# Kernel tuning notes

Measured on AMD Instinct MI355X. Metric: run time of the kernel, lower is better.

## Reference

```python
import jax, jax.numpy as jnp
import numpy as np

B, S, D, H = 2, 2048, 1024, 16
DK = D // H


def setup_inputs() -> dict:
    key = jax.random.key(0)
    ks = jax.random.split(key, 9)
    sc = 0.02
    return {
        "x": jax.random.normal(ks[0], (B, S, D), dtype=jnp.float32),
        "attention_mask": jnp.ones((B, S), dtype=jnp.int32),
        "Wq": jax.random.normal(ks[1], (D, D), dtype=jnp.float32) * sc,
        "bq": jax.random.normal(ks[2], (D,), dtype=jnp.float32) * sc,
        "Wk": jax.random.normal(ks[3], (D, D), dtype=jnp.float32) * sc,
        "bk": jax.random.normal(ks[4], (D,), dtype=jnp.float32) * sc,
        "Wv": jax.random.normal(ks[5], (D, D), dtype=jnp.float32) * sc,
        "bv": jax.random.normal(ks[6], (D,), dtype=jnp.float32) * sc,
        "Wo": jax.random.normal(ks[7], (D, D), dtype=jnp.float32) * sc,
        "bo": jax.random.normal(ks[8], (D,), dtype=jnp.float32) * sc,
    }


def reference(x, attention_mask, Wq, bq, Wk, bk, Wv, bv, Wo, bo):
    b, s, d = x.shape
    # projections (Linear: x @ W + b) then split heads -> [b, h, s, dk]
    def heads(t):
        return t.reshape(b, s, H, DK).transpose(0, 2, 1, 3)
    Q = heads(x @ Wq + bq)
    K = heads(x @ Wk + bk)
    V = heads(x @ Wv + bv)
    # NOTE: original computes K @ Q^T (not Q @ K^T) and applies NO 1/sqrt(dk) scale
    scores = jnp.einsum("bhid,bhjd->bhij", K, Q)  # [b, h, s, s]
    causal = jnp.tril(jnp.ones((s, s), dtype=bool))  # [s, s]
    final_mask = attention_mask[:, None, None, :].astype(bool) & causal[None, None]
    scores = jnp.where(final_mask, scores, -jnp.inf)
    attn = jax.nn.softmax(scores, axis=-1)
    out = jnp.einsum("bhij,bhjd->bhid", attn, V)  # [b, h, s, dk]
    out = out.transpose(0, 2, 1, 3).reshape(b, s, d)
    return out @ Wo + bo
```

## Files before the change

### kernel.cpp

```cpp
#include <hip/hip_runtime.h>
#include <stdint.h>
#include <stddef.h>


typedef short bf16x8 __attribute__((ext_vector_type(8)));
typedef float f32x4  __attribute__((ext_vector_type(4)));

__device__ __forceinline__ short f2bf(float f) {
  union { float f; uint32_t u; } a; a.f = f;
  uint32_t r = a.u + 0x7fffu + ((a.u >> 16) & 1u);
  return (short)(r >> 16);
}
__device__ __forceinline__ short f2bf_trunc(float f) {
  union { float f; uint32_t u; } a; a.f = f;
  return (short)(a.u >> 16);
}
__device__ __forceinline__ float bf2f(short s) {
  union { uint32_t u; float f; } a; a.u = ((uint32_t)(uint16_t)s) << 16;
  return a.f;
}
__device__ __forceinline__ float fast_exp2(float x) {
#if __has_builtin(__builtin_amdgcn_exp2f)
  return __builtin_amdgcn_exp2f(x);
#else
  return exp2f(x);
#endif
}
__device__ __forceinline__ void async16(const void* g, void* l) {
  __builtin_amdgcn_global_load_lds(
      (const __attribute__((address_space(1))) uint32_t*)g,
      (__attribute__((address_space(3))) uint32_t*)l, 16, 0, 0);
}
#define MFMA(a, b, c) __builtin_amdgcn_mfma_f32_16x16x32_bf16((a), (b), (c), 0, 0, 0)

__global__ void k_split_x(const float* __restrict__ x, short* __restrict__ xhi,
                          short* __restrict__ xlo) {
  int i = blockIdx.x * 256 + threadIdx.x;
  float4 v = ((const float4*)x)[i];
  short4 h, l;
  h.x = f2bf(v.x); l.x = f2bf(v.x - bf2f(h.x));
  h.y = f2bf(v.y); l.y = f2bf(v.y - bf2f(h.y));
  h.z = f2bf(v.z); l.z = f2bf(v.z - bf2f(h.z));
  h.w = f2bf(v.w); l.w = f2bf(v.w - bf2f(h.w));
  ((short4*)xhi)[i] = h;
  ((short4*)xlo)[i] = l;
}

__global__ void k_prep_w(const float* __restrict__ Wq, const float* __restrict__ Wk,
                         const float* __restrict__ Wv, const float* __restrict__ Wo,
                         short* __restrict__ whi) {
  __shared__ float T[64][65];
  int z = blockIdx.z;
  const float* W = (z == 0) ? Wq : (z == 1) ? Wk : (z == 2) ? Wv : Wo;
  int n0 = blockIdx.x * 64, k0 = blockIdx.y * 64;
  int t = threadIdx.x;
  int rr = t >> 4, cc = (t & 15) * 4;
#pragma unroll
  for (int it = 0; it < 4; ++it) {
    int row = rr + it * 16;
    float4 v = *(const float4*)&W[(size_t)(k0 + row) * 1024 + n0 + cc];
    T[row][cc] = v.x; T[row][cc + 1] = v.y; T[row][cc + 2] = v.z; T[row][cc + 3] = v.w;
  }
  __syncthreads();
  short* oh = whi + (size_t)z * 1048576;
#pragma unroll
  for (int it = 0; it < 4; ++it) {
    int nrow = rr + it * 16;
    short4 h4;
    h4.x = f2bf(T[cc + 0][nrow]);
    h4.y = f2bf(T[cc + 1][nrow]);
    h4.z = f2bf(T[cc + 2][nrow]);
    h4.w = f2bf(T[cc + 3][nrow]);
    *(short4*)&oh[(size_t)(n0 + nrow) * 1024 + k0 + cc] = h4;
  }
}

__global__ __launch_bounds__(256, 3) void k_gemm_qkv(
    const short* __restrict__ xhi, const short* __restrict__ xlo,
    const short* __restrict__ whi,
    const float* __restrict__ bq, const float* __restrict__ bk,
    const float* __restrict__ bv,
    short* __restrict__ Qhi, short* __restrict__ Qlo,
    short* __restrict__ Khi, short* __restrict__ Klo,
    short* __restrict__ Vb) {
  __shared__ short AH[2][4096];
  __shared__ short AL[2][4096];
  __shared__ short BH[2][4096];
  int tid = threadIdx.x;
  int bx = blockIdx.x;
  int m0 = blockIdx.y * 128;
  int n0g = bx * 128;
  bool SPLIT = (bx < 16);
  int w = tid >> 6, lane = tid & 63, lr = lane & 15, lq = lane >> 4;
  int wm = w >> 1, wn = w & 1;
  f32x4 acc[4][4] = {};

  auto stage = [&](int ks, int pb) {
#pragma unroll
    for (int it = 0; it < 2; ++it) {
      int idx = it * 256 + tid;
      int row = idx >> 2, c = idx & 3;
      int cs = c ^ (row & 3);
      size_t ga = (size_t)(m0 + row) * 1024 + ks * 32 + cs * 8;
      async16(xhi + ga, &AH[pb][idx * 8]);
      if (SPLIT) async16(xlo + ga, &AL[pb][idx * 8]);
      size_t gb = (size_t)(n0g + row) * 1024 + ks * 32 + cs * 8;
      async16(whi + gb, &BH[pb][idx * 8]);
    }
  };

  stage(0, 0);
  int p = 0;
  int g = lq ^ (lr & 3);
  for (int ks = 0; ks < 32; ++ks) {
    __syncthreads();
    if (ks < 31) stage(ks + 1, p ^ 1);
    const bf16x8* A8 = (const bf16x8*)AH[p];
    const bf16x8* L8 = (const bf16x8*)AL[p];
    const bf16x8* B8 = (const bf16x8*)BH[p];
    bf16x8 af[4], al[4], bfr[4];
#pragma unroll
    for (int mt = 0; mt < 4; ++mt) af[mt] = A8[(wm * 64 + mt * 16 + lr) * 4 + g];
#pragma unroll
    for (int nt = 0; nt < 4; ++nt) bfr[nt] = B8[(wn * 64 + nt * 16 + lr) * 4 + g];
    if (SPLIT) {
#pragma unroll
      for (int mt = 0; mt < 4; ++mt) al[mt] = L8[(wm * 64 + mt * 16 + lr) * 4 + g];
    }
#pragma unroll
    for (int mt = 0; mt < 4; ++mt)
#pragma unroll
      for (int nt = 0; nt < 4; ++nt)
        acc[mt][nt] = MFMA(af[mt], bfr[nt], acc[mt][nt]);
    if (SPLIT) {
#pragma unroll
      for (int mt = 0; mt < 4; ++mt)
#pragma unroll
        for (int nt = 0; nt < 4; ++nt)
          acc[mt][nt] = MFMA(al[mt], bfr[nt], acc[mt][nt]);
    }
    p ^= 1;
  }

  int z = bx >> 3;
  const float* bias = (z == 0) ? bq : (z == 1) ? bk : bv;
  short* Ch = (z == 0) ? Qhi : (z == 1) ? Khi : Vb;
  short* Cl = (z == 0) ? Qlo : Klo;
#pragma unroll
  for (int nt = 0; nt < 4; ++nt) {
    int colg = (n0g & 1023) + wn * 64 + nt * 16 + lr;
    float bvv = bias[colg];
#pragma unroll
    for (int mt = 0; mt < 4; ++mt)
#pragma unroll
      for (int r = 0; r < 4; ++r) {
        int row = m0 + wm * 64 + mt * 16 + lq * 4 + r;
        float v = acc[mt][nt][r] + bvv;
        size_t o = (size_t)row * 1024 + colg;
        if (z < 2) {
          short hh = f2bf(v);
          Ch[o] = hh;
          Cl[o] = f2bf(v - bf2f(hh));
        } else {
          Ch[o] = f2bf(v);
        }
      }
  }
}

__global__ __launch_bounds__(256, 2) void k_gemm_o(
    const short* __restrict__ Ab, const short* __restrict__ Bb,
    const float* __restrict__ bias, float* __restrict__ Cf) {
  __shared__ short AH[2][4096];
  __shared__ short BH[2][4096];
  int tid = threadIdx.x;
  int m0 = blockIdx.y * 128, n0 = blockIdx.x * 128;
  int w = tid >> 6, lane = tid & 63, lr = lane & 15, lq = lane >> 4;
  int wm = w >> 1, wn = w & 1;
  f32x4 acc[4][4] = {};

  auto stage = [&](int ks, int pb) {
#pragma unroll
    for (int it = 0; it < 2; ++it) {
      int idx = it * 256 + tid;
      int row = idx >> 2, c = idx & 3;
      int cs = c ^ (row & 3);
      async16(Ab + (size_t)(m0 + row) * 1024 + ks * 32 + cs * 8, &AH[pb][idx * 8]);
      async16(Bb + (size_t)(n0 + row) * 1024 + ks * 32 + cs * 8, &BH[pb][idx * 8]);
    }
  };

  stage(0, 0);
  int p = 0;
  int g = lq ^ (lr & 3);
  for (int ks = 0; ks < 32; ++ks) {
    __syncthreads();
    if (ks < 31) stage(ks + 1, p ^ 1);
    const bf16x8* A8 = (const bf16x8*)AH[p];
    const bf16x8* B8 = (const bf16x8*)BH[p];
    bf16x8 af[4], bfr[4];
#pragma unroll
    for (int mt = 0; mt < 4; ++mt) af[mt] = A8[(wm * 64 + mt * 16 + lr) * 4 + g];
#pragma unroll
    for (int nt = 0; nt < 4; ++nt) bfr[nt] = B8[(wn * 64 + nt * 16 + lr) * 4 + g];
#pragma unroll
    for (int mt = 0; mt < 4; ++mt)
#pragma unroll
      for (int nt = 0; nt < 4; ++nt)
        acc[mt][nt] = MFMA(af[mt], bfr[nt], acc[mt][nt]);
    p ^= 1;
  }
#pragma unroll
  for (int nt = 0; nt < 4; ++nt) {
    int col = n0 + wn * 64 + nt * 16 + lr;
    float bvv = bias[col];
#pragma unroll
    for (int mt = 0; mt < 4; ++mt)
#pragma unroll
      for (int r = 0; r < 4; ++r) {
        int row = m0 + wm * 64 + mt * 16 + lq * 4 + r;
        Cf[(size_t)row * 1024 + col] = acc[mt][nt][r] + bvv;
      }
  }
}

__global__ void k_vt(const short* __restrict__ Vb, short* __restrict__ Vt) {
  __shared__ short T[64][72];
  int s0 = blockIdx.x * 64;
  int bh = blockIdx.y, b = bh >> 4, h = bh & 15;
  int tid = threadIdx.x;
#pragma unroll
  for (int it = 0; it < 2; ++it) {
    int idx = it * 256 + tid, r = idx >> 3, c = idx & 7;
    bf16x8 v = *(const bf16x8*)(Vb + (size_t)(b * 2048 + s0 + r) * 1024 + h * 64 + c * 8);
    *(bf16x8*)&T[r][c * 8] = v;
  }
  __syncthreads();
#pragma unroll
  for (int it = 0; it < 2; ++it) {
    int idx = it * 256 + tid, d = idx >> 3, sc = idx & 7;
    bf16x8 vv;
#pragma unroll
    for (int j = 0; j < 8; ++j) vv[j] = T[sc * 8 + j][d];
    *(bf16x8*)(Vt + (size_t)(bh * 64 + d) * 2048 + s0 + sc * 8) = vv;
  }
}

__global__ __launch_bounds__(256, 2) void k_attn(
    const short* __restrict__ Khi, const short* __restrict__ Klo,
    const short* __restrict__ Qhi, const short* __restrict__ Qlo,
    const short* __restrict__ Vt, const int* __restrict__ amask,
    short* __restrict__ Obuf) {
  __shared__ short KQh[2][4096];
  __shared__ short KQl[2][4096];
  __shared__ short VS[2][4096];
  __shared__ short P[8][16 * 72];
  __shared__ float mb[2048];
  int tid = threadIdx.x;
  int pr = blockIdx.x;
  int bh = blockIdx.y, b = bh >> 4, h = bh & 15;
  int w = tid >> 6, lane = tid & 63, lr = lane & 15, lq = lane >> 4;
  const float LOG2E = 1.44269504f;
  int iA = pr, iB = 31 - pr;

  for (int j = tid; j < 2048; j += 256)
    mb[j] = amask[b * 2048 + j] ? 0.0f : -1e30f;

  bf16x8 qhA[2], qlA[2], qhB[2], qlB[2];
  {
    size_t ra = ((size_t)(b * 2048 + iA * 64 + w * 16 + lr)) * 1024 + h * 64;
    size_t rb = ((size_t)(b * 2048 + iB * 64 + w * 16 + lr)) * 1024 + h * 64;
#pragma unroll
    for (int ks = 0; ks < 2; ++ks) {
      qhA[ks] = *(const bf16x8*)(Khi + ra + ks * 32 + lq * 8);
      qlA[ks] = *(const bf16x8*)(Klo + ra + ks * 32 + lq * 8);
      qhB[ks] = *(const bf16x8*)(Khi + rb + ks * 32 + lq * 8);
      qlB[ks] = *(const bf16x8*)(Klo + rb + ks * 32 + lq * 8);
    }
  }

  f32x4 OA[4] = {}, OB[4] = {};
  float lsA[4] = {0.f, 0.f, 0.f, 0.f}, lsB[4] = {0.f, 0.f, 0.f, 0.f};
  int ibaseA = iA * 64 + w * 16 + lq * 4;
  int ibaseB = iB * 64 + w * 16 + lq * 4;
  int g = lq ^ (lr & 3);

  auto stage = [&](int jt, int pb) {
#pragma unroll
    for (int it = 0; it < 2; ++it) {
      int idx = it * 256 + tid;
      int rg = idx >> 8, rr = (idx >> 2) & 63, c = idx & 3;
      int cs = c ^ (rr & 3);
      size_t gq = ((size_t)(b * 2048 + jt * 64 + rr)) * 1024 + h * 64 + rg * 32 + cs * 8;
      async16(Qhi + gq, &KQh[pb][idx * 8]);
      async16(Qlo + gq, &KQl[pb][idx * 8]);
      size_t gv = ((size_t)(bh * 64 + rr)) * 2048 + jt * 64 + rg * 32 + cs * 8;
      async16(Vt + gv, &VS[pb][idx * 8]);
    }
  };

  auto softmax = [&](f32x4* s, float* ls, int ibase, int j0, bool diag, int slot) {
    float pv[4][4];
#pragma unroll
    for (int nt = 0; nt < 4; ++nt) {
      int j = j0 + nt * 16 + lr;
      float bias_j = mb[j];
#pragma unroll
      for (int r = 0; r < 4; ++r)
        pv[nt][r] = fast_exp2(s[nt][r] * LOG2E + bias_j);
    }
    if (diag) {
#pragma unroll
      for (int nt = 0; nt < 4; ++nt) {
        int j = j0 + nt * 16 + lr;
#pragma unroll
        for (int r = 0; r < 4; ++r)
          if (j > ibase + r) pv[nt][r] = 0.f;
      }
    }
#pragma unroll
    for (int nt = 0; nt < 4; ++nt)
#pragma unroll
      for (int r = 0; r < 4; ++r) {
        ls[r] += pv[nt][r];
        P[w * 2 + slot][(lq * 4 + r) * 72 + nt * 16 + lr] = f2bf_trunc(pv[nt][r]);
      }
  };

  stage(0, 0);
  int p = 0;
  for (int jt = 0; jt <= iB; ++jt) {
    __syncthreads();
    if (jt < iB) stage(jt + 1, p ^ 1);
    bool DUAL = (jt <= iA);
    int j0 = jt * 64;
    const bf16x8* KH8 = (const bf16x8*)KQh[p];
    const bf16x8* KL8 = (const bf16x8*)KQl[p];
    const bf16x8* V8  = (const bf16x8*)VS[p];

    f32x4 sA[4] = {}, sB[4] = {};
#pragma unroll
    for (int nt = 0; nt < 4; ++nt) {
      int ri = (nt * 16 + lr) * 4 + g;
#pragma unroll
      for (int ks = 0; ks < 2; ++ks) {
        bf16x8 kb  = KH8[ks * 256 + ri];
        bf16x8 klb = KL8[ks * 256 + ri];
        sB[nt] = MFMA(qhB[ks], kb, sB[nt]);
        sB[nt] = MFMA(qhB[ks], klb, sB[nt]);
        sB[nt] = MFMA(qlB[ks], kb, sB[nt]);
        if (DUAL) {
          sA[nt] = MFMA(qhA[ks], kb, sA[nt]);
          sA[nt] = MFMA(qhA[ks], klb, sA[nt]);
          sA[nt] = MFMA(qlA[ks], kb, sA[nt]);
        }
      }
    }
    softmax(sB, lsB, ibaseB, j0, jt == iB, 0);
    if (DUAL) softmax(sA, lsA, ibaseA, j0, jt == iA, 1);

    bf16x8 paB[2], paA[2];
#pragma unroll
    for (int ks = 0; ks < 2; ++ks)
      paB[ks] = *(const bf16x8*)&P[w * 2 + 0][lr * 72 + ks * 32 + lq * 8];
    if (DUAL) {
#pragma unroll
      for (int ks = 0; ks < 2; ++ks)
        paA[ks] = *(const bf16x8*)&P[w * 2 + 1][lr * 72 + ks * 32 + lq * 8];
    }
#pragma unroll
    for (int ks = 0; ks < 2; ++ks)
#pragma unroll
      for (int nt = 0; nt < 4; ++nt) {
        bf16x8 vb = V8[ks * 256 + (nt * 16 + lr) * 4 + g];
        OB[nt] = MFMA(paB[ks], vb, OB[nt]);
        if (DUAL) OA[nt] = MFMA(paA[ks], vb, OA[nt]);
      }
    p ^= 1;
  }

  auto fin = [&](f32x4* O, float* ls, int i0) {
#pragma unroll
    for (int r = 0; r < 4; ++r) {
      float t = ls[r];
      t += __shfl_xor(t, 1);
      t += __shfl_xor(t, 2);
      t += __shfl_xor(t, 4);
      t += __shfl_xor(t, 8);
      float inv = 1.0f / t;
#pragma unroll
      for (int nt = 0; nt < 4; ++nt) {
        int row = b * 2048 + i0 + w * 16 + lq * 4 + r;
        int col = h * 64 + nt * 16 + lr;
        Obuf[(size_t)row * 1024 + col] = f2bf(O[nt][r] * inv);
      }
    }
  };
  fin(OA, lsA, iA * 64);
  fin(OB, lsB, iB * 64);
}

extern "C" void kernel_launch(void* const* d_in, const int* in_sizes, int n_in,
                              void* d_out, int out_size, void* d_ws, size_t ws_size,
                              hipStream_t stream) {
  const float* x  = (const float*)d_in[0];
  const int* amask = (const int*)d_in[1];
  const float* Wq = (const float*)d_in[2];
  const float* bq = (const float*)d_in[3];
  const float* Wk = (const float*)d_in[4];
  const float* bk = (const float*)d_in[5];
  const float* Wv = (const float*)d_in[6];
  const float* bv = (const float*)d_in[7];
  const float* Wo = (const float*)d_in[8];
  const float* bo = (const float*)d_in[9];

  char* ws = (char*)d_ws;
  const size_t MB = 1024 * 1024;
  short* xhi = (short*)(ws);
  short* xlo = (short*)(ws + 8 * MB);
  short* whi = (short*)(ws + 16 * MB);
  short* Qhi = (short*)(ws + 28 * MB);
  short* Qlo = (short*)(ws + 36 * MB);
  short* Khi = (short*)(ws + 44 * MB);
  short* Klo = (short*)(ws + 52 * MB);
  short* Vb  = (short*)(ws + 60 * MB);
  short* Vt   = xhi;
  short* Obuf = xlo;

  k_split_x<<<4096, 256, 0, stream>>>(x, xhi, xlo);
  k_prep_w<<<dim3(16, 16, 4), 256, 0, stream>>>(Wq, Wk, Wv, Wo, whi);

  k_gemm_qkv<<<dim3(24, 32), 256, 0, stream>>>(xhi, xlo, whi, bq, bk, bv,
                                               Qhi, Qlo, Khi, Klo, Vb);
  k_vt<<<dim3(32, 32), 256, 0, stream>>>(Vb, Vt);
  k_attn<<<dim3(16, 32), 256, 0, stream>>>(Khi, Klo, Qhi, Qlo, Vt, amask, Obuf);
  k_gemm_o<<<dim3(8, 32), 256, 0, stream>>>(Obuf, whi + 3 * 1048576, bo, (float*)d_out);
}
```

Before: 251.7 us.

## Restructure attention to one band per block with transposed scores and register P

The attention kernel now handles a single 64-row band per block, longest bands first, instead of pairing bands A/B. It computes scores transposed so the softmax probabilities stay in registers and are reshuffled with ds_bpermute instead of going through an LDS P buffer. The mask is read per tile with a ballot fast path that skips masking when all keys are valid. LOG2E is folded into Q in the projection epilogue. Dropping the shared P and mask buffers allows three blocks per CU, at the cost of losing the pairwise load balancing and adding cross-lane permutes.

```diff
diff --git a/kernel.cpp b/kernel.cpp
--- a/kernel.cpp
+++ b/kernel.cpp
@@ -11,13 +11,13 @@
   uint32_t r = a.u + 0x7fffu + ((a.u >> 16) & 1u);
   return (short)(r >> 16);
 }
-__device__ __forceinline__ short f2bf_trunc(float f) {
-  union { float f; uint32_t u; } a; a.f = f;
-  return (short)(a.u >> 16);
-}
 __device__ __forceinline__ float bf2f(short s) {
   union { uint32_t u; float f; } a; a.u = ((uint32_t)(uint16_t)s) << 16;
   return a.f;
+}
+__device__ __forceinline__ uint32_t pack2bf(float a, float b) {
+  union { float f; uint32_t u; } x, y; x.f = a; y.f = b;
+  return (x.u >> 16) | (y.u & 0xffff0000u);
 }
 __device__ __forceinline__ float fast_exp2(float x) {
 #if __has_builtin(__builtin_amdgcn_exp2f)
@@ -143,6 +143,7 @@
   }
 
   int z = bx >> 3;
+  const float LOG2E = 1.44269504f;
   const float* bias = (z == 0) ? bq : (z == 1) ? bk : bv;
   short* Ch = (z == 0) ? Qhi : (z == 1) ? Khi : Vb;
   short* Cl = (z == 0) ? Qlo : Klo;
@@ -156,6 +157,7 @@
       for (int r = 0; r < 4; ++r) {
         int row = m0 + wm * 64 + mt * 16 + lq * 4 + r;
         float v = acc[mt][nt][r] + bvv;
+        if (z == 0) v *= LOG2E;
         size_t o = (size_t)row * 1024 + colg;
         if (z < 2) {
           short hh = f2bf(v);
@@ -246,158 +248,142 @@
   }
 }
 
-__global__ __launch_bounds__(256, 2) void k_attn(
+__global__ __launch_bounds__(256, 3) void k_attn(
     const short* __restrict__ Khi, const short* __restrict__ Klo,
     const short* __restrict__ Qhi, const short* __restrict__ Qlo,
     const short* __restrict__ Vt, const int* __restrict__ amask,
     short* __restrict__ Obuf) {
-  __shared__ short KQh[2][4096];
-  __shared__ short KQl[2][4096];
+  __shared__ short QH[2][4096];
+  __shared__ short QL[2][4096];
   __shared__ short VS[2][4096];
-  __shared__ short P[8][16 * 72];
-  __shared__ float mb[2048];
   int tid = threadIdx.x;
-  int pr = blockIdx.x;
+  int band = 31 - blockIdx.x;
   int bh = blockIdx.y, b = bh >> 4, h = bh & 15;
   int w = tid >> 6, lane = tid & 63, lr = lane & 15, lq = lane >> 4;
-  const float LOG2E = 1.44269504f;
-  int iA = pr, iB = 31 - pr;
-
-  for (int j = tid; j < 2048; j += 256)
-    mb[j] = amask[b * 2048 + j] ? 0.0f : -1e30f;
-
-  bf16x8 qhA[2], qlA[2], qhB[2], qlB[2];
+  int i0 = band * 64;
+
+  bf16x8 kh[2], kl[2];
   {
-    size_t ra = ((size_t)(b * 2048 + iA * 64 + w * 16 + lr)) * 1024 + h * 64;
-    size_t rb = ((size_t)(b * 2048 + iB * 64 + w * 16 + lr)) * 1024 + h * 64;
+    size_t ra = ((size_t)(b * 2048 + i0 + w * 16 + lr)) * 1024 + h * 64;
 #pragma unroll
     for (int ks = 0; ks < 2; ++ks) {
-      qhA[ks] = *(const bf16x8*)(Khi + ra + ks * 32 + lq * 8);
-      qlA[ks] = *(const bf16x8*)(Klo + ra + ks * 32 + lq * 8);
-      qhB[ks] = *(const bf16x8*)(Khi + rb + ks * 32 + lq * 8);
-      qlB[ks] = *(const bf16x8*)(Klo + rb + ks * 32 + lq * 8);
-    }
-  }
-
-  f32x4 OA[4] = {}, OB[4] = {};
-  float lsA[4] = {0.f, 0.f, 0.f, 0.f}, lsB[4] = {0.f, 0.f, 0.f, 0.f};
-  int ibaseA = iA * 64 + w * 16 + lq * 4;
-  int ibaseB = iB * 64 + w * 16 + lq * 4;
-  int g = lq ^ (lr & 3);
+      kh[ks] = *(const bf16x8*)(Khi + ra + ks * 32 + lq * 8);
+      kl[ks] = *(const bf16x8*)(Klo + ra + ks * 32 + lq * 8);
+    }
+  }
+
+  f32x4 O[4] = {};
+  float lsacc = 0.f;
+  int iq = i0 + w * 16 + lr;
+  int baddr0 = (((lq & 1) * 2) * 16 + lr) * 4;
+  int baddr1 = baddr0 + 64;
 
   auto stage = [&](int jt, int pb) {
+    int j0 = jt * 64;
 #pragma unroll
     for (int it = 0; it < 2; ++it) {
       int idx = it * 256 + tid;
-      int rg = idx >> 8, rr = (idx >> 2) & 63, c = idx & 3;
-      int cs = c ^ (rr & 3);
-      size_t gq = ((size_t)(b * 2048 + jt * 64 + rr)) * 1024 + h * 64 + rg * 32 + cs * 8;
-      async16(Qhi + gq, &KQh[pb][idx * 8]);
-      async16(Qlo + gq, &KQl[pb][idx * 8]);
-      size_t gv = ((size_t)(bh * 64 + rr)) * 2048 + jt * 64 + rg * 32 + cs * 8;
+      int rr = idx >> 3, c = idx & 7;
+      int cs = c ^ (rr & 7);
+      size_t gq = ((size_t)(b * 2048 + j0 + rr)) * 1024 + h * 64 + cs * 8;
+      async16(Qhi + gq, &QH[pb][idx * 8]);
+      async16(Qlo + gq, &QL[pb][idx * 8]);
+      size_t gv = ((size_t)(bh * 64 + rr)) * 2048 + j0 + cs * 8;
       async16(Vt + gv, &VS[pb][idx * 8]);
     }
-  };
-
-  auto softmax = [&](f32x4* s, float* ls, int ibase, int j0, bool diag, int slot) {
-    float pv[4][4];
-#pragma unroll
-    for (int nt = 0; nt < 4; ++nt) {
-      int j = j0 + nt * 16 + lr;
-      float bias_j = mb[j];
-#pragma unroll
-      for (int r = 0; r < 4; ++r)
-        pv[nt][r] = fast_exp2(s[nt][r] * LOG2E + bias_j);
-    }
-    if (diag) {
-#pragma unroll
-      for (int nt = 0; nt < 4; ++nt) {
-        int j = j0 + nt * 16 + lr;
-#pragma unroll
-        for (int r = 0; r < 4; ++r)
-          if (j > ibase + r) pv[nt][r] = 0.f;
-      }
-    }
-#pragma unroll
-    for (int nt = 0; nt < 4; ++nt)
-#pragma unroll
-      for (int r = 0; r < 4; ++r) {
-        ls[r] += pv[nt][r];
-        P[w * 2 + slot][(lq * 4 + r) * 72 + nt * 16 + lr] = f2bf_trunc(pv[nt][r]);
-      }
   };
 
   stage(0, 0);
   int p = 0;
-  for (int jt = 0; jt <= iB; ++jt) {
+  for (int jt = 0; jt <= band; ++jt) {
     __syncthreads();
-    if (jt < iB) stage(jt + 1, p ^ 1);
-    bool DUAL = (jt <= iA);
+    if (jt < band) stage(jt + 1, p ^ 1);
     int j0 = jt * 64;
-    const bf16x8* KH8 = (const bf16x8*)KQh[p];
-    const bf16x8* KL8 = (const bf16x8*)KQl[p];
-    const bf16x8* V8  = (const bf16x8*)VS[p];
-
-    f32x4 sA[4] = {}, sB[4] = {};
-#pragma unroll
-    for (int nt = 0; nt < 4; ++nt) {
-      int ri = (nt * 16 + lr) * 4 + g;
+    const bf16x8* Q8 = (const bf16x8*)QH[p];
+    const bf16x8* L8 = (const bf16x8*)QL[p];
+    const bf16x8* V8 = (const bf16x8*)VS[p];
+
+    int av = amask[b * 2048 + j0 + lane];
+    unsigned long long bal = __ballot(av != 0);
+    bool allv = (bal == ~0ull);
+
+    f32x4 s[4] = {};
+#pragma unroll
+    for (int mt = 0; mt < 4; ++mt) {
+      int row = mt * 16 + lr;
 #pragma unroll
       for (int ks = 0; ks < 2; ++ks) {
-        bf16x8 kb  = KH8[ks * 256 + ri];
-        bf16x8 klb = KL8[ks * 256 + ri];
-        sB[nt] = MFMA(qhB[ks], kb, sB[nt]);
-        sB[nt] = MFMA(qhB[ks], klb, sB[nt]);
-        sB[nt] = MFMA(qlB[ks], kb, sB[nt]);
-        if (DUAL) {
-          sA[nt] = MFMA(qhA[ks], kb, sA[nt]);
-          sA[nt] = MFMA(qhA[ks], klb, sA[nt]);
-          sA[nt] = MFMA(qlA[ks], kb, sA[nt]);
-        }
+        int gi = row * 8 + ((ks * 4 + lq) ^ (row & 7));
+        bf16x8 qa = Q8[gi];
+        bf16x8 la = L8[gi];
+        s[mt] = MFMA(qa, kh[ks], s[mt]);
+        s[mt] = MFMA(la, kh[ks], s[mt]);
+        s[mt] = MFMA(qa, kl[ks], s[mt]);
       }
     }
-    softmax(sB, lsB, ibaseB, j0, jt == iB, 0);
-    if (DUAL) softmax(sA, lsA, ibaseA, j0, jt == iA, 1);
-
-    bf16x8 paB[2], paA[2];
-#pragma unroll
-    for (int ks = 0; ks < 2; ++ks)
-      paB[ks] = *(const bf16x8*)&P[w * 2 + 0][lr * 72 + ks * 32 + lq * 8];
-    if (DUAL) {
-#pragma unroll
-      for (int ks = 0; ks < 2; ++ks)
-        paA[ks] = *(const bf16x8*)&P[w * 2 + 1][lr * 72 + ks * 32 + lq * 8];
-    }
-#pragma unroll
-    for (int ks = 0; ks < 2; ++ks)
+
+    float pv[4][4];
+#pragma unroll
+    for (int mt = 0; mt < 4; ++mt)
+#pragma unroll
+      for (int r = 0; r < 4; ++r)
+        pv[mt][r] = fast_exp2(s[mt][r]);
+    if (jt == band) {
+#pragma unroll
+      for (int mt = 0; mt < 4; ++mt)
+#pragma unroll
+        for (int r = 0; r < 4; ++r)
+          if (j0 + mt * 16 + lq * 4 + r > iq) pv[mt][r] = 0.f;
+    }
+    if (!allv) {
+#pragma unroll
+      for (int mt = 0; mt < 4; ++mt)
+#pragma unroll
+        for (int r = 0; r < 4; ++r)
+          if (!((bal >> (mt * 16 + lq * 4 + r)) & 1)) pv[mt][r] = 0.f;
+    }
+    uint32_t pd[4][2];
+#pragma unroll
+    for (int mt = 0; mt < 4; ++mt) {
+      lsacc += (pv[mt][0] + pv[mt][1]) + (pv[mt][2] + pv[mt][3]);
+      pd[mt][0] = pack2bf(pv[mt][0], pv[mt][1]);
+      pd[mt][1] = pack2bf(pv[mt][2], pv[mt][3]);
+    }
+
+#pragma unroll
+    for (int k2 = 0; k2 < 2; ++k2) {
+      union { int i[4]; bf16x8 v; } pa;
+#pragma unroll
+      for (int dd = 0; dd < 4; ++dd) {
+        int addr = (dd >> 1) ? baddr1 : baddr0;
+        int v0 = __builtin_amdgcn_ds_bpermute(addr, (int)pd[k2 * 2 + 0][dd & 1]);
+        int v1 = __builtin_amdgcn_ds_bpermute(addr, (int)pd[k2 * 2 + 1][dd & 1]);
+        pa.i[dd] = (lq >> 1) ? v1 : v0;
+      }
 #pragma unroll
       for (int nt = 0; nt < 4; ++nt) {
-        bf16x8 vb = V8[ks * 256 + (nt * 16 + lr) * 4 + g];
-        OB[nt] = MFMA(paB[ks], vb, OB[nt]);
-        if (DUAL) OA[nt] = MFMA(paA[ks], vb, OA[nt]);
+        int row = nt * 16 + lr;
+        bf16x8 vb = V8[row * 8 + ((k2 * 4 + lq) ^ (row & 7))];
+        O[nt] = MFMA(pa.v, vb, O[nt]);
       }
+    }
     p ^= 1;
   }
 
-  auto fin = [&](f32x4* O, float* ls, int i0) {
+  float t = lsacc;
+  t += __shfl_xor(t, 16);
+  t += __shfl_xor(t, 32);
+  float inv[4];
+#pragma unroll
+  for (int r = 0; r < 4; ++r) inv[r] = 1.0f / __shfl(t, lq * 4 + r, 64);
+#pragma unroll
+  for (int nt = 0; nt < 4; ++nt)
 #pragma unroll
     for (int r = 0; r < 4; ++r) {
-      float t = ls[r];
-      t += __shfl_xor(t, 1);
-      t += __shfl_xor(t, 2);
-      t += __shfl_xor(t, 4);
-      t += __shfl_xor(t, 8);
-      float inv = 1.0f / t;
-#pragma unroll
-      for (int nt = 0; nt < 4; ++nt) {
-        int row = b * 2048 + i0 + w * 16 + lq * 4 + r;
-        int col = h * 64 + nt * 16 + lr;
-        Obuf[(size_t)row * 1024 + col] = f2bf(O[nt][r] * inv);
-      }
-    }
-  };
-  fin(OA, lsA, iA * 64);
-  fin(OB, lsB, iB * 64);
+      int row = b * 2048 + i0 + w * 16 + lq * 4 + r;
+      int col = h * 64 + nt * 16 + lr;
+      Obuf[(size_t)row * 1024 + col] = f2bf(O[nt][r] * inv[r]);
+    }
 }
 
 extern "C" void kernel_launch(void* const* d_in, const int* in_sizes, int n_in,
@@ -433,6 +419,6 @@
   k_gemm_qkv<<<dim3(24, 32), 256, 0, stream>>>(xhi, xlo, whi, bq, bk, bv,
                                                Qhi, Qlo, Khi, Klo, Vb);
   k_vt<<<dim3(32, 32), 256, 0, stream>>>(Vb, Vt);
-  k_attn<<<dim3(16, 32), 256, 0, stream>>>(Khi, Klo, Qhi, Qlo, Vt, amask, Obuf);
+  k_attn<<<dim3(32, 32), 256, 0, stream>>>(Khi, Klo, Qhi, Qlo, Vt, amask, Obuf);
   k_gemm_o<<<dim3(8, 32), 256, 0, stream>>>(Obuf, whi + 3 * 1048576, bo, (float*)d_out);
 }
```

After: 289.5 us. 1.15x slower.
